# Optimization experiments

Hardware: AMD Instinct MI355X
Metric: run time of the kernel (lower is better)

The kernel has to match this reference:

```python
import jax, jax.numpy as jnp
import numpy as np

N_NODES = 100000
N_EDGES = 1600000
IN_FEAT = 64
OUT_FEAT = 64
K_ORDER = 1
BN_EPS = 1e-5


def setup_inputs() -> dict:
    key = jax.random.key(0)
    ks = jax.random.split(key, 8)
    feature = jax.random.normal(ks[0], (N_NODES, IN_FEAT), dtype=jnp.float32)
    sp_embeddings = jax.random.normal(ks[1], (N_NODES, 16), dtype=jnp.float32)
    edge_src = jax.random.randint(ks[2], (N_EDGES,), 0, N_NODES, dtype=jnp.int32)
    edge_dst = jax.random.randint(ks[3], (N_EDGES,), 0, N_NODES, dtype=jnp.int32)
    edge_order = jax.random.randint(ks[4], (N_EDGES,), 0, K_ORDER + 1, dtype=jnp.int32)
    # xavier_normal over (in, out) fan dims
    std = float(np.sqrt(2.0 / (IN_FEAT + OUT_FEAT)))
    linear = jax.random.normal(ks[5], (K_ORDER + 1, IN_FEAT, OUT_FEAT), dtype=jnp.float32) * std
    mlp_w = jax.random.normal(ks[6], (OUT_FEAT, OUT_FEAT), dtype=jnp.float32) * std
    mlp_b = jnp.zeros((OUT_FEAT,), dtype=jnp.float32)
    bn_gamma = jnp.ones((OUT_FEAT,), dtype=jnp.float32)
    bn_beta = jnp.zeros((OUT_FEAT,), dtype=jnp.float32)
    return {
        "feature": feature,
        "sp_embeddings": sp_embeddings,
        "linear": linear,
        "mlp_w": mlp_w,
        "mlp_b": mlp_b,
        "bn_gamma": bn_gamma,
        "bn_beta": bn_beta,
        "edge_src": edge_src,
        "edge_dst": edge_dst,
        "edge_order": edge_order,
    }


def reference(feature, sp_embeddings, linear, mlp_w, mlp_b, bn_gamma, bn_beta,
              edge_src, edge_dst, edge_order):
    # msg_fun: gather per-edge weight matrix by edge order, batched matvec
    W_e = linear[edge_order]          # [E, in, out]
    h_src = feature[edge_src]          # [E, in]
    msg = jnp.einsum('eio,ei->eo', W_e, h_src)  # [E, out]
    # agg_fun: scatter-sum messages into destination nodes
    h = jax.ops.segment_sum(msg, edge_dst, num_segments=N_NODES)  # [N, out]
    # mlp: Linear -> ReLU -> BatchNorm1d (training mode: batch stats)
    h = jax.nn.relu(h @ mlp_w.T + mlp_b)
    mean = jnp.mean(h, axis=0)
    var = jnp.var(h, axis=0)  # biased, matching torch BN normalization
    h = (h - mean) * jax.lax.rsqrt(var + BN_EPS) * bn_gamma + bn_beta
    # shortcut=False -> no residual; sp_embeddings unused by forward
    return h
```

## Files before the change

kernel.cpp:

```cpp
#include <hip/hip_runtime.h>

#define N_NODES 100000
#define N_EDGES 1600000
#define NBUCK 1563
#define NBLK 256
#define PER_BLK 6250
#define MAX_BE 2048


__device__ __forceinline__ unsigned short f2bf(float x) {
  unsigned u = __float_as_uint(x);
  unsigned r = (u + 0x7FFFu + ((u >> 16) & 1u)) >> 16;
  return (unsigned short)r;
}

__global__ __launch_bounds__(256) void prep_U(const float* __restrict__ linear,
                                              const float* __restrict__ mlp_w,
                                              float* __restrict__ U) {
  int idx = blockIdx.x * 256 + threadIdx.x;
  int o = idx & 63;
  int ki = idx >> 6;
  int k = ki >> 6, i = ki & 63;
  float acc = 0.f;
#pragma unroll 8
  for (int j = 0; j < 64; ++j)
    acc += linear[ki * 64 + j] * mlp_w[o * 64 + j];
  U[i * 128 + k * 64 + o] = acc;
}

__global__ __launch_bounds__(256) void prep_B(const float* __restrict__ feature,
                                              const float* __restrict__ U,
                                              unsigned short* __restrict__ B) {
  __shared__ float Us[64 * 128];
  for (int i = threadIdx.x; i < 64 * 128; i += 256) Us[i] = U[i];
  __syncthreads();
  const int ra = blockIdx.x * 512 + threadIdx.x;
  const int rb = ra + 256;
  const bool va = ra < N_NODES, vb = rb < N_NODES;
  const float4* Fa = reinterpret_cast<const float4*>(feature + (size_t)(va ? ra : 0) * 64);
  const float4* Fb = reinterpret_cast<const float4*>(feature + (size_t)(vb ? rb : 0) * 64);
#pragma unroll
  for (int k = 0; k < 2; ++k) {
    float acc0[64], acc1[64];
#pragma unroll
    for (int o = 0; o < 64; ++o) { acc0[o] = 0.f; acc1[o] = 0.f; }
#pragma unroll 2
    for (int i4 = 0; i4 < 16; ++i4) {
      float4 a = Fa[i4];
      float4 cc = Fb[i4];
      float av[4] = {a.x, a.y, a.z, a.w};
      float cv[4] = {cc.x, cc.y, cc.z, cc.w};
#pragma unroll
      for (int u = 0; u < 4; ++u) {
        const float* Ur = &Us[(i4 * 4 + u) * 128 + k * 64];
#pragma unroll
        for (int o = 0; o < 64; ++o) {
          float w = Ur[o];
          acc0[o] = fmaf(av[u], w, acc0[o]);
          acc1[o] = fmaf(cv[u], w, acc1[o]);
        }
      }
    }
    if (va) {
      ushort4* Bp = reinterpret_cast<ushort4*>(B + (((size_t)ra * 2 + k) << 6));
#pragma unroll
      for (int o4 = 0; o4 < 16; ++o4) {
        ushort4 pk;
        pk.x = f2bf(acc0[o4 * 4 + 0]);
        pk.y = f2bf(acc0[o4 * 4 + 1]);
        pk.z = f2bf(acc0[o4 * 4 + 2]);
        pk.w = f2bf(acc0[o4 * 4 + 3]);
        Bp[o4] = pk;
      }
    }
    if (vb) {
      ushort4* Bp = reinterpret_cast<ushort4*>(B + (((size_t)rb * 2 + k) << 6));
#pragma unroll
      for (int o4 = 0; o4 < 16; ++o4) {
        ushort4 pk;
        pk.x = f2bf(acc1[o4 * 4 + 0]);
        pk.y = f2bf(acc1[o4 * 4 + 1]);
        pk.z = f2bf(acc1[o4 * 4 + 2]);
        pk.w = f2bf(acc1[o4 * 4 + 3]);
        Bp[o4] = pk;
      }
    }
  }
}

__global__ __launch_bounds__(512) void countA(const int* __restrict__ edst,
                                              unsigned* __restrict__ cntg) {
  __shared__ unsigned h[NBUCK];
  for (int i = threadIdx.x; i < NBUCK; i += 512) h[i] = 0;
  __syncthreads();
  const int k = blockIdx.x;
  const int beg = k * PER_BLK, end = beg + PER_BLK;
  for (int e = beg + (int)threadIdx.x; e < end; e += 512)
    atomicAdd(&h[((unsigned)edst[e]) >> 6], 1u);
  __syncthreads();
  for (int i = threadIdx.x; i < NBUCK; i += 512)
    cntg[(size_t)k * NBUCK + i] = h[i];
}

__global__ __launch_bounds__(256) void scanT1(unsigned* __restrict__ cntg,
                                              unsigned* __restrict__ tot) {
  const int lane = threadIdx.x & 63;
  const int wv = threadIdx.x >> 6;
  const int b = blockIdx.x * 4 + wv;
  if (b >= NBUCK) return;
  unsigned c[4];
  unsigned lsum = 0;
#pragma unroll
  for (int j = 0; j < 4; ++j) {
    c[j] = cntg[(size_t)(lane * 4 + j) * NBUCK + b];
    lsum += c[j];
  }
  unsigned inc = lsum;
#pragma unroll
  for (int d = 1; d < 64; d <<= 1) {
    unsigned n = __shfl_up(inc, d);
    if (lane >= d) inc += n;
  }
  unsigned run = inc - lsum;
#pragma unroll
  for (int j = 0; j < 4; ++j) {
    cntg[(size_t)(lane * 4 + j) * NBUCK + b] = run;
    run += c[j];
  }
  unsigned total = __shfl(inc, 63);
  if (lane == 0) tot[b] = total;
}

__global__ __launch_bounds__(256) void scanT2(const unsigned* __restrict__ tot,
                                              unsigned* __restrict__ base) {
  __shared__ unsigned sh[256];
  const int t = threadIdx.x;
  unsigned local[7];
  unsigned s = 0;
#pragma unroll
  for (int i = 0; i < 7; ++i) {
    int idx = t * 7 + i;
    local[i] = (idx < NBUCK) ? tot[idx] : 0u;
    s += local[i];
  }
  sh[t] = s;
  __syncthreads();
#pragma unroll
  for (int off = 1; off < 256; off <<= 1) {
    unsigned v = (t >= off) ? sh[t - off] : 0u;
    __syncthreads();
    sh[t] += v;
    __syncthreads();
  }
  unsigned run = sh[t] - s;
#pragma unroll
  for (int i = 0; i < 7; ++i) {
    int idx = t * 7 + i;
    if (idx < NBUCK) { base[idx] = run; run += local[i]; }
  }
  if (t == 0) base[NBUCK] = N_EDGES;
}

__global__ __launch_bounds__(512) void fillB(const int* __restrict__ esrc,
                                             const int* __restrict__ edst,
                                             const int* __restrict__ eord,
                                             const unsigned* __restrict__ cntg,
                                             const unsigned* __restrict__ base,
                                             unsigned* __restrict__ pay) {
  __shared__ unsigned curL[NBUCK];
  const int k = blockIdx.x;
  for (int i = threadIdx.x; i < NBUCK; i += 512)
    curL[i] = base[i] + cntg[(size_t)k * NBUCK + i];
  __syncthreads();
  const int beg = k * PER_BLK, end = beg + PER_BLK;
  for (int e = beg + (int)threadIdx.x; e < end; e += 512) {
    unsigned d = (unsigned)edst[e];
    unsigned pos = atomicAdd(&curL[d >> 6], 1u);
    pay[pos] = ((d & 63u) << 18) | ((unsigned)esrc[e] << 1) | (unsigned)eord[e];
  }
}

__global__ __launch_bounds__(256) void bgather(const unsigned* __restrict__ base,
                                               const unsigned* __restrict__ pay,
                                               const unsigned short* __restrict__ B,
                                               const float* __restrict__ bias,
                                               float* __restrict__ out,
                                               double* __restrict__ stats) {
  __shared__ unsigned hist[64];
  __shared__ unsigned offsL[65];
  __shared__ unsigned curN[64];
  __shared__ unsigned pay_s[MAX_BE];
  __shared__ double dd0[4][64];
  __shared__ double dd1[4][64];
  const int tid = threadIdx.x;
  const int lane = tid & 63;
  const int wv = tid >> 6;
  const int b = blockIdx.x;
  const unsigned base0 = base[b];
  const unsigned n_e = base[b + 1] - base0;

  if (tid < 64) hist[tid] = 0;
  __syncthreads();
  for (unsigned i = tid; i < n_e; i += 256)
    atomicAdd(&hist[pay[base0 + i] >> 18], 1u);
  __syncthreads();
  if (wv == 0) {
    unsigned hv = hist[lane];
    unsigned inc = hv;
#pragma unroll
    for (int d = 1; d < 64; d <<= 1) {
      unsigned n = __shfl_up(inc, d);
      if (lane >= d) inc += n;
    }
    offsL[lane + 1] = inc;
    if (lane == 0) offsL[0] = 0;
    curN[lane] = inc - hv;
  }
  __syncthreads();
  for (unsigned i = tid; i < n_e; i += 256) {
    unsigned w = pay[base0 + i];
    unsigned pos = atomicAdd(&curN[w >> 18], 1u);
    pay_s[pos] = w;
  }
  __syncthreads();

  const int g = tid >> 4;
  const int sl = tid & 15;
  const int c0 = sl << 2;
  const float4 bo4 = *reinterpret_cast<const float4*>(bias + c0);
  double s0[4] = {0, 0, 0, 0}, s1[4] = {0, 0, 0, 0};

#pragma unroll
  for (int i = 0; i < 4; ++i) {
    const int nl = (g << 2) + i;
    const int ng = (b << 6) + nl;
    unsigned e = offsL[nl];
    const unsigned e1 = offsL[nl + 1];
    float s[4] = {0.f, 0.f, 0.f, 0.f};
    while (e < e1) {
      unsigned rem = e1 - e;
      int cnt = rem < 8u ? (int)rem : 8;
      unsigned p[8];
      uint2 v[8];
#pragma unroll
      for (int j = 0; j < 8; ++j)
        p[j] = pay_s[e + (j < cnt ? (unsigned)j : 0u)];
#pragma unroll
      for (int j = 0; j < 8; ++j)
        v[j] = *reinterpret_cast<const uint2*>(
            B + (((size_t)(p[j] & 0x3FFFFu)) << 6) + c0);
#pragma unroll
      for (int j = 0; j < 8; ++j) {
        if (j < cnt) {
          s[0] += __uint_as_float(v[j].x << 16);
          s[1] += __uint_as_float(v[j].x & 0xFFFF0000u);
          s[2] += __uint_as_float(v[j].y << 16);
          s[3] += __uint_as_float(v[j].y & 0xFFFF0000u);
        }
      }
      e += cnt;
    }
    if (ng < N_NODES) {
      float4 r;
      r.x = fmaxf(s[0] + bo4.x, 0.f);
      r.y = fmaxf(s[1] + bo4.y, 0.f);
      r.z = fmaxf(s[2] + bo4.z, 0.f);
      r.w = fmaxf(s[3] + bo4.w, 0.f);
      *reinterpret_cast<float4*>(out + ((size_t)ng << 6) + c0) = r;
      s0[0] += (double)r.x; s1[0] += (double)r.x * (double)r.x;
      s0[1] += (double)r.y; s1[1] += (double)r.y * (double)r.y;
      s0[2] += (double)r.z; s1[2] += (double)r.z * (double)r.z;
      s0[3] += (double)r.w; s1[3] += (double)r.w * (double)r.w;
    }
  }

#pragma unroll
  for (int q = 0; q < 4; ++q) {
    double v0 = s0[q], v1 = s1[q];
    v0 += __shfl_xor(v0, 16); v0 += __shfl_xor(v0, 32);
    v1 += __shfl_xor(v1, 16); v1 += __shfl_xor(v1, 32);
    s0[q] = v0; s1[q] = v1;
  }
  if ((lane & 48) == 0) {
#pragma unroll
    for (int q = 0; q < 4; ++q) {
      dd0[wv][c0 + q] = s0[q];
      dd1[wv][c0 + q] = s1[q];
    }
  }
  __syncthreads();
  if (tid < 64) {
    double t0 = dd0[0][tid] + dd0[1][tid] + dd0[2][tid] + dd0[3][tid];
    double t1 = dd1[0][tid] + dd1[1][tid] + dd1[2][tid] + dd1[3][tid];
    atomicAdd(&stats[tid], t0);
    atomicAdd(&stats[64 + tid], t1);
  }
}

__global__ __launch_bounds__(256) void bn_apply(float* __restrict__ h,
                                                const double* __restrict__ stats,
                                                const float* __restrict__ gamma,
                                                const float* __restrict__ beta) {
  const int lane = threadIdx.x & 63;
  double mean = stats[lane] * (1.0 / N_NODES);
  double var = stats[64 + lane] * (1.0 / N_NODES) - mean * mean;
  float inv = (float)(1.0 / sqrt(var + 1e-5));
  float scale = gamma[lane] * inv;
  float shift = beta[lane] - (float)mean * scale;
  int wid = (blockIdx.x * 256 + threadIdx.x) >> 6;
  const int nw = gridDim.x * 4;
  for (int r = wid; r < N_NODES; r += nw) {
    size_t idx = ((size_t)r << 6) + lane;
    h[idx] = h[idx] * scale + shift;
  }
}

extern "C" void kernel_launch(void* const* d_in, const int* in_sizes, int n_in,
                              void* d_out, int out_size, void* d_ws, size_t ws_size,
                              hipStream_t stream) {
  const float* feature = (const float*)d_in[0];
  const float* linear = (const float*)d_in[2];
  const float* mlp_w  = (const float*)d_in[3];
  const float* mlp_b  = (const float*)d_in[4];
  const float* gamma  = (const float*)d_in[5];
  const float* beta   = (const float*)d_in[6];
  const int* esrc = (const int*)d_in[7];
  const int* edst = (const int*)d_in[8];
  const int* eord = (const int*)d_in[9];
  float* out = (float*)d_out;

  char* basep = (char*)d_ws;
  unsigned*       cntg  = (unsigned*)(basep);
  unsigned*       tot   = (unsigned*)(basep + 1600512);
  unsigned*       base  = (unsigned*)(basep + 1606768);
  double*         stats = (double*)  (basep + 1613056);
  float*          U     = (float*)   (basep + 1614080);
  unsigned*       pay   = (unsigned*)(basep + 1646848);
  unsigned short* B     = (unsigned short*)(basep + 8046848);

  (void)hipMemsetAsync(stats, 0, 1024, stream);
  prep_U<<<32, 256, 0, stream>>>(linear, mlp_w, U);
  countA<<<NBLK, 512, 0, stream>>>(edst, cntg);
  scanT1<<<(NBUCK + 3) / 4, 256, 0, stream>>>(cntg, tot);
  scanT2<<<1, 256, 0, stream>>>(tot, base);
  fillB<<<NBLK, 512, 0, stream>>>(esrc, edst, eord, cntg, base, pay);
  prep_B<<<(N_NODES + 511) / 512, 256, 0, stream>>>(feature, U, B);
  bgather<<<NBUCK, 256, 0, stream>>>(base, pay, B, mlp_b, out, stats);
  bn_apply<<<1024, 256, 0, stream>>>(out, stats, gamma, beta);
}
```

Baseline: 168.6 us.

## Replace global bucket scans with per-partition local offsets read by bgather

Removes the two global scan kernels and instead computes a per-partition exclusive scan of bucket counts inside fillB, writing payloads into each partition's own region. bgather now reads, per thread, the segment for its bucket from one source partition using a 2D offset table. This cuts two launches and the strided global scan, at the cost of uncoalesced per-thread serial reads of small segments and strided offset-table loads in bgather.

After: 181.9 us. +7.9%, slower.

```diff
diff --git a/kernel.cpp b/kernel.cpp
--- a/kernel.cpp
+++ b/kernel.cpp
@@ -5,6 +5,7 @@
 #define NBUCK 1563
 #define NBLK 256
 #define PER_BLK 6250
+#define ROWLEN 1564
 #define MAX_BE 2048
 
 
@@ -102,85 +103,64 @@
     cntg[(size_t)k * NBUCK + i] = h[i];
 }
 
-__global__ __launch_bounds__(256) void scanT1(unsigned* __restrict__ cntg,
-                                              unsigned* __restrict__ tot) {
-  const int lane = threadIdx.x & 63;
-  const int wv = threadIdx.x >> 6;
-  const int b = blockIdx.x * 4 + wv;
-  if (b >= NBUCK) return;
-  unsigned c[4];
-  unsigned lsum = 0;
-#pragma unroll
-  for (int j = 0; j < 4; ++j) {
-    c[j] = cntg[(size_t)(lane * 4 + j) * NBUCK + b];
-    lsum += c[j];
-  }
-  unsigned inc = lsum;
-#pragma unroll
-  for (int d = 1; d < 64; d <<= 1) {
-    unsigned n = __shfl_up(inc, d);
-    if (lane >= d) inc += n;
-  }
-  unsigned run = inc - lsum;
-#pragma unroll
-  for (int j = 0; j < 4; ++j) {
-    cntg[(size_t)(lane * 4 + j) * NBUCK + b] = run;
-    run += c[j];
-  }
-  unsigned total = __shfl(inc, 63);
-  if (lane == 0) tot[b] = total;
-}
-
-__global__ __launch_bounds__(256) void scanT2(const unsigned* __restrict__ tot,
-                                              unsigned* __restrict__ base) {
-  __shared__ unsigned sh[256];
-  const int t = threadIdx.x;
-  unsigned local[7];
-  unsigned s = 0;
-#pragma unroll
-  for (int i = 0; i < 7; ++i) {
-    int idx = t * 7 + i;
-    local[i] = (idx < NBUCK) ? tot[idx] : 0u;
-    s += local[i];
-  }
-  sh[t] = s;
-  __syncthreads();
-#pragma unroll
-  for (int off = 1; off < 256; off <<= 1) {
-    unsigned v = (t >= off) ? sh[t - off] : 0u;
-    __syncthreads();
-    sh[t] += v;
-    __syncthreads();
-  }
-  unsigned run = sh[t] - s;
-#pragma unroll
-  for (int i = 0; i < 7; ++i) {
-    int idx = t * 7 + i;
-    if (idx < NBUCK) { base[idx] = run; run += local[i]; }
-  }
-  if (t == 0) base[NBUCK] = N_EDGES;
-}
-
 __global__ __launch_bounds__(512) void fillB(const int* __restrict__ esrc,
                                              const int* __restrict__ edst,
                                              const int* __restrict__ eord,
                                              const unsigned* __restrict__ cntg,
-                                             const unsigned* __restrict__ base,
+                                             unsigned* __restrict__ pfx2,
                                              unsigned* __restrict__ pay) {
-  __shared__ unsigned curL[NBUCK];
+  __shared__ unsigned cur[NBUCK];
+  __shared__ unsigned wtot[8];
   const int k = blockIdx.x;
-  for (int i = threadIdx.x; i < NBUCK; i += 512)
-    curL[i] = base[i] + cntg[(size_t)k * NBUCK + i];
-  __syncthreads();
-  const int beg = k * PER_BLK, end = beg + PER_BLK;
-  for (int e = beg + (int)threadIdx.x; e < end; e += 512) {
+  const int tid = threadIdx.x;
+  const int lane = tid & 63;
+  const int wv = tid >> 6;
+
+  unsigned loc[4];
+  unsigned s = 0;
+#pragma unroll
+  for (int j = 0; j < 4; ++j) {
+    int idx = tid * 4 + j;
+    loc[j] = (idx < NBUCK) ? cntg[(size_t)k * NBUCK + idx] : 0u;
+    s += loc[j];
+  }
+  unsigned inc = s;
+#pragma unroll
+  for (int d = 1; d < 64; d <<= 1) {
+    unsigned n = __shfl_up(inc, d);
+    if (lane >= d) inc += n;
+  }
+  if (lane == 63) wtot[wv] = inc;
+  __syncthreads();
+  if (tid == 0) {
+    unsigned r = 0;
+#pragma unroll
+    for (int w = 0; w < 8; ++w) { unsigned t = wtot[w]; wtot[w] = r; r += t; }
+  }
+  __syncthreads();
+  unsigned run = wtot[wv] + (inc - s);
+#pragma unroll
+  for (int j = 0; j < 4; ++j) {
+    int idx = tid * 4 + j;
+    if (idx < NBUCK) {
+      pfx2[(size_t)k * ROWLEN + idx] = run;
+      cur[idx] = run;
+      run += loc[j];
+    }
+  }
+  if (tid == 0) pfx2[(size_t)k * ROWLEN + NBUCK] = PER_BLK;
+  __syncthreads();
+
+  const int beg = k * PER_BLK;
+  for (int e = beg + tid; e < beg + PER_BLK; e += 512) {
     unsigned d = (unsigned)edst[e];
-    unsigned pos = atomicAdd(&curL[d >> 6], 1u);
-    pay[pos] = ((d & 63u) << 18) | ((unsigned)esrc[e] << 1) | (unsigned)eord[e];
-  }
-}
-
-__global__ __launch_bounds__(256) void bgather(const unsigned* __restrict__ base,
+    unsigned pos = atomicAdd(&cur[d >> 6], 1u);
+    pay[(size_t)beg + pos] =
+        ((d & 63u) << 18) | ((unsigned)esrc[e] << 1) | (unsigned)eord[e];
+  }
+}
+
+__global__ __launch_bounds__(256) void bgather(const unsigned* __restrict__ pfx2,
                                                const unsigned* __restrict__ pay,
                                                const unsigned short* __restrict__ B,
                                                const float* __restrict__ bias,
@@ -196,13 +176,14 @@
   const int lane = tid & 63;
   const int wv = tid >> 6;
   const int b = blockIdx.x;
-  const unsigned base0 = base[b];
-  const unsigned n_e = base[b + 1] - base0;
 
   if (tid < 64) hist[tid] = 0;
-  __syncthreads();
-  for (unsigned i = tid; i < n_e; i += 256)
-    atomicAdd(&hist[pay[base0 + i] >> 18], 1u);
+  const unsigned st = pfx2[(size_t)tid * ROWLEN + b];
+  const unsigned en = pfx2[(size_t)tid * ROWLEN + b + 1];
+  const unsigned regbase = (unsigned)tid * PER_BLK;
+  __syncthreads();
+  for (unsigned j = st; j < en; ++j)
+    atomicAdd(&hist[pay[regbase + j] >> 18], 1u);
   __syncthreads();
   if (wv == 0) {
     unsigned hv = hist[lane];
@@ -217,8 +198,8 @@
     curN[lane] = inc - hv;
   }
   __syncthreads();
-  for (unsigned i = tid; i < n_e; i += 256) {
-    unsigned w = pay[base0 + i];
+  for (unsigned j = st; j < en; ++j) {
+    unsigned w = pay[regbase + j];
     unsigned pos = atomicAdd(&curN[w >> 18], 1u);
     pay_s[pos] = w;
   }
@@ -331,20 +312,17 @@
 
   char* basep = (char*)d_ws;
   unsigned*       cntg  = (unsigned*)(basep);
-  unsigned*       tot   = (unsigned*)(basep + 1600512);
-  unsigned*       base  = (unsigned*)(basep + 1606768);
-  double*         stats = (double*)  (basep + 1613056);
-  float*          U     = (float*)   (basep + 1614080);
-  unsigned*       pay   = (unsigned*)(basep + 1646848);
-  unsigned short* B     = (unsigned short*)(basep + 8046848);
+  unsigned*       pfx2  = (unsigned*)(basep + 1600512);
+  double*         stats = (double*)  (basep + 3202048);
+  float*          U     = (float*)   (basep + 3203072);
+  unsigned*       pay   = (unsigned*)(basep + 3235840);
+  unsigned short* B     = (unsigned short*)(basep + 9635840);
 
   (void)hipMemsetAsync(stats, 0, 1024, stream);
   prep_U<<<32, 256, 0, stream>>>(linear, mlp_w, U);
   countA<<<NBLK, 512, 0, stream>>>(edst, cntg);
-  scanT1<<<(NBUCK + 3) / 4, 256, 0, stream>>>(cntg, tot);
-  scanT2<<<1, 256, 0, stream>>>(tot, base);
-  fillB<<<NBLK, 512, 0, stream>>>(esrc, edst, eord, cntg, base, pay);
+  fillB<<<NBLK, 512, 0, stream>>>(esrc, edst, eord, cntg, pfx2, pay);
   prep_B<<<(N_NODES + 511) / 512, 256, 0, stream>>>(feature, U, B);
-  bgather<<<NBUCK, 256, 0, stream>>>(base, pay, B, mlp_b, out, stats);
+  bgather<<<NBUCK, 256, 0, stream>>>(pfx2, pay, B, mlp_b, out, stats);
   bn_apply<<<1024, 256, 0, stream>>>(out, stats, gamma, beta);
 }
```

## Halve destination buckets to 32 nodes, cache payload in LDS, vectorize BN apply

Applied to the files above, without the earlier changes.

Destination buckets shrink from 64 to 32 nodes, which doubles the number of bgather blocks and halves per-block work and shared-memory arrays. The count, scan and fill kernels and the workspace offsets are resized to match. bgather now keeps the bucket's payload in LDS during the histogram pass, so the scatter pass does not read it from global memory again. bn_apply processes float4 elements per thread instead of one scalar per lane. Costs are a larger count matrix and longer scans, plus dropping the node-bounds check because 100000 divides evenly by 32.

New measurement: 232.0 us. +37.6%, slower.

```diff
diff --git a/kernel.cpp b/kernel.cpp
--- a/kernel.cpp
+++ b/kernel.cpp
@@ -2,10 +2,10 @@
 
 #define N_NODES 100000
 #define N_EDGES 1600000
-#define NBUCK 1563
+#define NBUCK 3125
 #define NBLK 256
 #define PER_BLK 6250
-#define MAX_BE 2048
+#define MAX_BE 1024
 
 
 __device__ __forceinline__ unsigned short f2bf(float x) {
@@ -96,7 +96,7 @@
   const int k = blockIdx.x;
   const int beg = k * PER_BLK, end = beg + PER_BLK;
   for (int e = beg + (int)threadIdx.x; e < end; e += 512)
-    atomicAdd(&h[((unsigned)edst[e]) >> 6], 1u);
+    atomicAdd(&h[((unsigned)edst[e]) >> 5], 1u);
   __syncthreads();
   for (int i = threadIdx.x; i < NBUCK; i += 512)
     cntg[(size_t)k * NBUCK + i] = h[i];
@@ -135,11 +135,11 @@
                                               unsigned* __restrict__ base) {
   __shared__ unsigned sh[256];
   const int t = threadIdx.x;
-  unsigned local[7];
+  unsigned local[13];
   unsigned s = 0;
 #pragma unroll
-  for (int i = 0; i < 7; ++i) {
-    int idx = t * 7 + i;
+  for (int i = 0; i < 13; ++i) {
+    int idx = t * 13 + i;
     local[i] = (idx < NBUCK) ? tot[idx] : 0u;
     s += local[i];
   }
@@ -154,8 +154,8 @@
   }
   unsigned run = sh[t] - s;
 #pragma unroll
-  for (int i = 0; i < 7; ++i) {
-    int idx = t * 7 + i;
+  for (int i = 0; i < 13; ++i) {
+    int idx = t * 13 + i;
     if (idx < NBUCK) { base[idx] = run; run += local[i]; }
   }
   if (t == 0) base[NBUCK] = N_EDGES;
@@ -175,8 +175,8 @@
   const int beg = k * PER_BLK, end = beg + PER_BLK;
   for (int e = beg + (int)threadIdx.x; e < end; e += 512) {
     unsigned d = (unsigned)edst[e];
-    unsigned pos = atomicAdd(&curL[d >> 6], 1u);
-    pay[pos] = ((d & 63u) << 18) | ((unsigned)esrc[e] << 1) | (unsigned)eord[e];
+    unsigned pos = atomicAdd(&curL[d >> 5], 1u);
+    pay[pos] = ((d & 31u) << 18) | ((unsigned)esrc[e] << 1) | (unsigned)eord[e];
   }
 }
 
@@ -186,9 +186,10 @@
                                                const float* __restrict__ bias,
                                                float* __restrict__ out,
                                                double* __restrict__ stats) {
-  __shared__ unsigned hist[64];
-  __shared__ unsigned offsL[65];
-  __shared__ unsigned curN[64];
+  __shared__ unsigned hist[32];
+  __shared__ unsigned offsL[33];
+  __shared__ unsigned curN[32];
+  __shared__ unsigned pay_raw[MAX_BE];
   __shared__ unsigned pay_s[MAX_BE];
   __shared__ double dd0[4][64];
   __shared__ double dd1[4][64];
@@ -199,26 +200,31 @@
   const unsigned base0 = base[b];
   const unsigned n_e = base[b + 1] - base0;
 
-  if (tid < 64) hist[tid] = 0;
-  __syncthreads();
-  for (unsigned i = tid; i < n_e; i += 256)
-    atomicAdd(&hist[pay[base0 + i] >> 18], 1u);
+  if (tid < 32) hist[tid] = 0;
+  __syncthreads();
+  for (unsigned i = tid; i < n_e; i += 256) {
+    unsigned w = pay[base0 + i];
+    pay_raw[i] = w;
+    atomicAdd(&hist[w >> 18], 1u);
+  }
   __syncthreads();
   if (wv == 0) {
-    unsigned hv = hist[lane];
+    unsigned hv = (lane < 32) ? hist[lane] : 0u;
     unsigned inc = hv;
 #pragma unroll
-    for (int d = 1; d < 64; d <<= 1) {
+    for (int d = 1; d < 32; d <<= 1) {
       unsigned n = __shfl_up(inc, d);
       if (lane >= d) inc += n;
     }
-    offsL[lane + 1] = inc;
+    if (lane < 32) {
+      offsL[lane + 1] = inc;
+      curN[lane] = inc - hv;
+    }
     if (lane == 0) offsL[0] = 0;
-    curN[lane] = inc - hv;
   }
   __syncthreads();
   for (unsigned i = tid; i < n_e; i += 256) {
-    unsigned w = pay[base0 + i];
+    unsigned w = pay_raw[i];
     unsigned pos = atomicAdd(&curN[w >> 18], 1u);
     pay_s[pos] = w;
   }
@@ -231,9 +237,9 @@
   double s0[4] = {0, 0, 0, 0}, s1[4] = {0, 0, 0, 0};
 
 #pragma unroll
-  for (int i = 0; i < 4; ++i) {
-    const int nl = (g << 2) + i;
-    const int ng = (b << 6) + nl;
+  for (int i = 0; i < 2; ++i) {
+    const int nl = (g << 1) + i;
+    const int ng = (b << 5) + nl;
     unsigned e = offsL[nl];
     const unsigned e1 = offsL[nl + 1];
     float s[4] = {0.f, 0.f, 0.f, 0.f};
@@ -260,18 +266,16 @@
       }
       e += cnt;
     }
-    if (ng < N_NODES) {
-      float4 r;
-      r.x = fmaxf(s[0] + bo4.x, 0.f);
-      r.y = fmaxf(s[1] + bo4.y, 0.f);
-      r.z = fmaxf(s[2] + bo4.z, 0.f);
-      r.w = fmaxf(s[3] + bo4.w, 0.f);
-      *reinterpret_cast<float4*>(out + ((size_t)ng << 6) + c0) = r;
-      s0[0] += (double)r.x; s1[0] += (double)r.x * (double)r.x;
-      s0[1] += (double)r.y; s1[1] += (double)r.y * (double)r.y;
-      s0[2] += (double)r.z; s1[2] += (double)r.z * (double)r.z;
-      s0[3] += (double)r.w; s1[3] += (double)r.w * (double)r.w;
-    }
+    float4 r;
+    r.x = fmaxf(s[0] + bo4.x, 0.f);
+    r.y = fmaxf(s[1] + bo4.y, 0.f);
+    r.z = fmaxf(s[2] + bo4.z, 0.f);
+    r.w = fmaxf(s[3] + bo4.w, 0.f);
+    *reinterpret_cast<float4*>(out + ((size_t)ng << 6) + c0) = r;
+    s0[0] += (double)r.x; s1[0] += (double)r.x * (double)r.x;
+    s0[1] += (double)r.y; s1[1] += (double)r.y * (double)r.y;
+    s0[2] += (double)r.z; s1[2] += (double)r.z * (double)r.z;
+    s0[3] += (double)r.w; s1[3] += (double)r.w * (double)r.w;
   }
 
 #pragma unroll
@@ -301,17 +305,27 @@
                                                 const double* __restrict__ stats,
                                                 const float* __restrict__ gamma,
                                                 const float* __restrict__ beta) {
-  const int lane = threadIdx.x & 63;
-  double mean = stats[lane] * (1.0 / N_NODES);
-  double var = stats[64 + lane] * (1.0 / N_NODES) - mean * mean;
-  float inv = (float)(1.0 / sqrt(var + 1e-5));
-  float scale = gamma[lane] * inv;
-  float shift = beta[lane] - (float)mean * scale;
-  int wid = (blockIdx.x * 256 + threadIdx.x) >> 6;
-  const int nw = gridDim.x * 4;
-  for (int r = wid; r < N_NODES; r += nw) {
-    size_t idx = ((size_t)r << 6) + lane;
-    h[idx] = h[idx] * scale + shift;
+  const int idx0 = blockIdx.x * 256 + threadIdx.x;
+  const int cg = (idx0 & 15) << 2;
+  float sc[4], sh[4];
+#pragma unroll
+  for (int q = 0; q < 4; ++q) {
+    double mean = stats[cg + q] * (1.0 / N_NODES);
+    double var = stats[64 + cg + q] * (1.0 / N_NODES) - mean * mean;
+    float inv = (float)(1.0 / sqrt(var + 1e-5));
+    sc[q] = gamma[cg + q] * inv;
+    sh[q] = beta[cg + q] - (float)mean * sc[q];
+  }
+  float4* h4 = reinterpret_cast<float4*>(h);
+  const int total = N_NODES * 16;
+  const int stride = gridDim.x * 256;
+  for (int idx = idx0; idx < total; idx += stride) {
+    float4 v = h4[idx];
+    v.x = v.x * sc[0] + sh[0];
+    v.y = v.y * sc[1] + sh[1];
+    v.z = v.z * sc[2] + sh[2];
+    v.w = v.w * sc[3] + sh[3];
+    h4[idx] = v;
   }
 }
 
@@ -331,12 +345,12 @@
 
   char* basep = (char*)d_ws;
   unsigned*       cntg  = (unsigned*)(basep);
-  unsigned*       tot   = (unsigned*)(basep + 1600512);
-  unsigned*       base  = (unsigned*)(basep + 1606768);
-  double*         stats = (double*)  (basep + 1613056);
-  float*          U     = (float*)   (basep + 1614080);
-  unsigned*       pay   = (unsigned*)(basep + 1646848);
-  unsigned short* B     = (unsigned short*)(basep + 8046848);
+  unsigned*       tot   = (unsigned*)(basep + 3200000);
+  unsigned*       base  = (unsigned*)(basep + 3212500);
+  double*         stats = (double*)  (basep + 3225008);
+  float*          U     = (float*)   (basep + 3226032);
+  unsigned*       pay   = (unsigned*)(basep + 3258800);
+  unsigned short* B     = (unsigned short*)(basep + 9658800);
 
   (void)hipMemsetAsync(stats, 0, 1024, stream);
   prep_U<<<32, 256, 0, stream>>>(linear, mlp_w, U);
```
